# Kernel optimization log

Measured on AMD Instinct MI355X. Metric: run time of the kernel, lower is better.

## Reference

```python
import jax, jax.numpy as jnp
import numpy as np

N, E = 50000, 800000
IN_DIM, OUT_DIM, NHEAD = 256, 64, 4
SLOPE = 0.2
BN_EPS = 1e-5


def setup_inputs() -> dict:
    key = jax.random.key(0)
    ks = jax.random.split(key, 12)
    HD = NHEAD * OUT_DIM
    s = 1.0 / np.sqrt(IN_DIM)
    inp = {
        'feat': jax.random.normal(ks[0], (N, IN_DIM), dtype=jnp.float32),
        'src': jax.random.randint(ks[1], (E,), 0, N, dtype=jnp.int32),
        'dst': jax.random.randint(ks[2], (E,), 0, N, dtype=jnp.int32),
        # GATv2Conv params (DGL: separate src/dst linear, per-head attn vector, output bias)
        'W_src': jax.random.normal(ks[3], (IN_DIM, HD), dtype=jnp.float32) * s,
        'b_src': jnp.zeros((HD,), dtype=jnp.float32),
        'W_dst': jax.random.normal(ks[4], (IN_DIM, HD), dtype=jnp.float32) * s,
        'b_dst': jnp.zeros((HD,), dtype=jnp.float32),
        'attn': jax.random.normal(ks[5], (NHEAD, OUT_DIM), dtype=jnp.float32) * (1.0 / np.sqrt(OUT_DIM)),
        'out_bias': jnp.zeros((HD,), dtype=jnp.float32),
        # trailing fc: Linear(HD -> OUT_DIM) + BatchNorm1d + LeakyReLU (dropout = identity in eval)
        'fc_W': jax.random.normal(ks[6], (HD, OUT_DIM), dtype=jnp.float32) * (1.0 / np.sqrt(HD)),
        'fc_b': jnp.zeros((OUT_DIM,), dtype=jnp.float32),
        'gamma': jnp.ones((OUT_DIM,), dtype=jnp.float32),
        'beta': jnp.zeros((OUT_DIM,), dtype=jnp.float32),
    }
    return inp


def _leaky(x):
    return jnp.where(x >= 0, x, SLOPE * x)


def reference(feat, src, dst, W_src, b_src, W_dst, b_dst, attn, out_bias, fc_W, fc_b, gamma, beta):
    H, D = NHEAD, OUT_DIM
    h_src = (feat @ W_src + b_src).reshape(N, H, D)
    h_dst = (feat @ W_dst + b_dst).reshape(N, H, D)
    # per-edge GATv2 score: attn . LeakyReLU(h_src[u] + h_dst[v])
    hs_e = h_src[src]                                   # [E,H,D]
    e = jnp.einsum('ehd,hd->eh', _leaky(hs_e + h_dst[dst]), attn)  # [E,H]
    # segment softmax over incoming edges of each dst node
    m = jax.ops.segment_max(e, dst, num_segments=N)     # [N,H]
    ex = jnp.exp(e - m[dst])
    denom = jax.ops.segment_sum(ex, dst, num_segments=N)
    a = ex / denom[dst]                                 # [E,H]
    # weighted scatter-add aggregation
    rst = jax.ops.segment_sum(a[:, :, None] * hs_e, dst, num_segments=N)  # [N,H,D]
    rst = rst + out_bias.reshape(H, D)
    # trailing fc + BatchNorm1d (batch stats) + LeakyReLU
    z = rst.reshape(N, H * D) @ fc_W + fc_b
    mu = jnp.mean(z, axis=0)
    var = jnp.var(z, axis=0)
    z = (z - mu) * jax.lax.rsqrt(var + BN_EPS) * gamma + beta
    return _leaky(z)
```

## Files before the change

kernel.cpp:

```cpp
#include <hip/hip_runtime.h>
#include <math.h>

#define N_NODES 50000
#define N_EDGES 800000
#define HD 256
#define OUT_DIM 64
#define NHEAD 4
#define SLOPE 0.2f
#define BN_EPS 1e-5f
#define LOG2E 1.4426950408889634f
#define NTILES 391
#define HIST_BLOCKS 96

typedef __attribute__((ext_vector_type(8))) short short8;
typedef __attribute__((ext_vector_type(4))) float float4v;

__device__ __forceinline__ float leaky(float x) { return x >= 0.f ? x : SLOPE * x; }

__device__ __forceinline__ float bf2f(unsigned short u) {
    return __uint_as_float(((unsigned)u) << 16);
}
__device__ __forceinline__ unsigned short f2bf(float f) {
    unsigned u = __float_as_uint(f);
    unsigned r = (u + 0x7fffu + ((u >> 16) & 1u)) >> 16;
    return (unsigned short)r;
}

__device__ __forceinline__ short8 pack8(const float4 a, const float4 b) {
    short8 r;
    r[0] = (short)f2bf(a.x); r[1] = (short)f2bf(a.y);
    r[2] = (short)f2bf(a.z); r[3] = (short)f2bf(a.w);
    r[4] = (short)f2bf(b.x); r[5] = (short)f2bf(b.y);
    r[6] = (short)f2bf(b.z); r[7] = (short)f2bf(b.w);
    return r;
}

template <int CTRL>
__device__ __forceinline__ float ror_add(float v) {
    const int r = __builtin_amdgcn_update_dpp(0, __float_as_int(v), CTRL, 0xF, 0xF, true);
    return v + __int_as_float(r);
}
__device__ __forceinline__ float group16_sum(float v) {
    v = ror_add<0x121>(v);
    v = ror_add<0x122>(v);
    v = ror_add<0x124>(v);
    v = ror_add<0x128>(v);
    return v;
}

__global__ __launch_bounds__(256) void prep_kernel(const float* __restrict__ W_src,
                                                   const float* __restrict__ W_dst,
                                                   const float* __restrict__ fc_W,
                                                   unsigned short* __restrict__ WtS,
                                                   unsigned short* __restrict__ WtD,
                                                   unsigned short* __restrict__ WtF,
                                                   int* __restrict__ cnt2,
                                                   float* __restrict__ sums,
                                                   int* __restrict__ done) {
    const int b = blockIdx.x;
    const int t = threadIdx.x;
    if (b < 256) {
        WtS[(size_t)b * 256 + t] = f2bf(W_src[(size_t)t * 256 + b]);
    } else if (b < 512) {
        const int n = b - 256;
        WtD[(size_t)n * 256 + t] = f2bf(W_dst[(size_t)t * 256 + n]);
    } else if (b < 576) {
        const int n = b - 512;
        WtF[(size_t)n * 256 + t] = f2bf(fc_W[(size_t)t * 64 + n]);
    } else if (b < 674) {
        const int i = (b - 576) * 256 + t;
        if (i < 25000) ((int4*)cnt2)[i] = make_int4(0, 0, 0, 0);
    } else {
        if (t < 128) sums[t] = 0.f;
        if (t == 128) done[0] = 0;
    }
}

__global__ __launch_bounds__(256) void proj_kernel(const float* __restrict__ feat,
                                                   const unsigned short* __restrict__ BtS,
                                                   const unsigned short* __restrict__ BtD,
                                                   const float* __restrict__ bS,
                                                   const float* __restrict__ bD,
                                                   unsigned short* __restrict__ CS,
                                                   unsigned short* __restrict__ CD,
                                                   const int* __restrict__ dst,
                                                   int* __restrict__ cnt) {
    __shared__ unsigned short Bs[64 * 256];

    if (blockIdx.x < HIST_BLOCKS) {
        for (int i = blockIdx.x * 256 + threadIdx.x; i < N_EDGES; i += HIST_BLOCKS * 256)
            atomicAdd(&cnt[dst[i]], 1);
        return;
    }

    const int tile = blockIdx.x - HIST_BLOCKS;
    if (tile >= NTILES) return;

    const int t    = threadIdx.x;
    const int w    = t >> 6;
    const int lane = t & 63;
    const int q    = lane >> 4;
    const int l16  = lane & 15;

    const int m0 = tile * 128;

    int ar0 = m0 + w * 32 + l16;
    int ar1 = ar0 + 16;
    if (ar0 > N_NODES - 1) ar0 = N_NODES - 1;
    if (ar1 > N_NODES - 1) ar1 = N_NODES - 1;
    const float* Af0 = feat + (size_t)ar0 * 256 + q * 8;
    const float* Af1 = feat + (size_t)ar1 * 256 + q * 8;
    short8 afr0[8], afr1[8];
#pragma unroll
    for (int kk = 0; kk < 8; ++kk) {
        const float4 x0 = *(const float4*)(Af0 + kk * 32);
        const float4 y0 = *(const float4*)(Af0 + kk * 32 + 4);
        const float4 x1 = *(const float4*)(Af1 + kk * 32);
        const float4 y1 = *(const float4*)(Af1 + kk * 32 + 4);
        afr0[kk] = pack8(x0, y0);
        afr1[kk] = pack8(x1, y1);
    }

    const int r   = t >> 2;
    const int seg = t & 3;
    const int cc  = r >> 4;
    const int L   = r & 15;

    const int la8 = lane * 8;
    const int lsw[4] = {la8, la8 ^ 16, la8 ^ 32, la8 ^ 48};

    for (int ph = 0; ph < 8; ++ph) {
        const bool isD = (ph >= 4);
        const int  c0  = (ph & 3) * 64;
        const unsigned short* Bt   = isD ? BtD : BtS;
        const float*          bias = isD ? bD  : bS;
        unsigned short*       C    = isD ? CD  : CS;

        __syncthreads();
        {
            const unsigned short* g = Bt + (size_t)(c0 + r) * 256 + seg * 64;
#pragma unroll
            for (int kk2 = 0; kk2 < 2; ++kk2) {
                const int kk   = seg * 2 + kk2;
                const int c8kk = cc * 8 + kk;
                const int key  = ((c8kk >> 1) & 3) << 4;
#pragma unroll
                for (int q2 = 0; q2 < 4; ++q2)
                    *(short8*)(&Bs[((c8kk * 64 + q2 * 16 + L) * 8) ^ key]) =
                        *(const short8*)(g + kk2 * 32 + q2 * 8);
            }
        }
        __syncthreads();

        float vb[4];
#pragma unroll
        for (int c = 0; c < 4; ++c) vb[c] = bias[c0 + c * 16 + l16];

        float4v a0[4] = {}, a1[4] = {};
#pragma unroll
        for (int kk = 0; kk < 8; ++kk) {
            const short8 af0 = afr0[kk];
            const short8 af1 = afr1[kk];
#pragma unroll
            for (int c = 0; c < 4; ++c) {
                const int c8kk = c * 8 + kk;
                const short8 b = *(const short8*)(&Bs[c8kk * 512 + lsw[(c8kk >> 1) & 3]]);
                a0[c] = __builtin_amdgcn_mfma_f32_16x16x32_bf16(af0, b, a0[c], 0, 0, 0);
                a1[c] = __builtin_amdgcn_mfma_f32_16x16x32_bf16(af1, b, a1[c], 0, 0, 0);
            }
        }

        __syncthreads();
        unsigned short* Cw = Bs + w * 2304;
#pragma unroll
        for (int c = 0; c < 4; ++c) {
            const int cl = c * 16 + l16;
#pragma unroll
            for (int i = 0; i < 4; ++i) {
                Cw[(q * 4 + i) * 72 + cl]      = f2bf(a0[c][i] + vb[c]);
                Cw[(q * 4 + i + 16) * 72 + cl] = f2bf(a1[c][i] + vb[c]);
            }
        }
#pragma unroll
        for (int j = 0; j < 4; ++j) {
            const int rl = j * 8 + (lane >> 3);
            const short8 v = *(const short8*)(Cw + rl * 72 + (lane & 7) * 8);
            const int rg = m0 + w * 32 + rl;
            if (rg < N_NODES)
                *(short8*)(&C[(size_t)rg * 256 + c0 + (lane & 7) * 8]) = v;
        }
    }
}

__global__ __launch_bounds__(256) void fc_bn_kernel(const unsigned short* __restrict__ A,
                                                    const unsigned short* __restrict__ Bt,
                                                    const float* __restrict__ bias,
                                                    float* __restrict__ C,
                                                    float* __restrict__ sums,
                                                    int M) {
    const int w    = threadIdx.x >> 6;
    const int lane = threadIdx.x & 63;
    const int q    = lane >> 4;
    const int l16  = lane & 15;
    const int m0   = blockIdx.x * 64;
    const int t    = threadIdx.x;

    __shared__ float ssum[64], ssq[64];
    if (t < 64) { ssum[t] = 0.f; ssq[t] = 0.f; }

    int arow = m0 + w * 16 + l16;
    if (arow > M - 1) arow = M - 1;
    const unsigned short* Ab  = A  + (size_t)arow * 256 + q * 8;
    const unsigned short* Btb = Bt + (size_t)l16 * 256 + q * 8;

    float4v acc[4] = {};

    for (int k0 = 0; k0 < 256; k0 += 32) {
        const short8 af = *(const short8*)(Ab + k0);
#pragma unroll
        for (int c = 0; c < 4; ++c) {
            const short8 bf = *(const short8*)(Btb + (size_t)c * 16 * 256 + k0);
            acc[c] = __builtin_amdgcn_mfma_f32_16x16x32_bf16(af, bf, acc[c], 0, 0, 0);
        }
    }
    __syncthreads();

#pragma unroll
    for (int c = 0; c < 4; ++c) {
        const int col = c * 16 + l16;
        const float b = bias[col];
        float s = 0.f, qq = 0.f;
#pragma unroll
        for (int i = 0; i < 4; ++i) {
            const int r = m0 + w * 16 + q * 4 + i;
            if (r < M) {
                const float v = acc[c][i] + b;
                C[(size_t)r * 64 + col] = v;
                s += v;
                qq += v * v;
            }
        }
        atomicAdd(&ssum[col], s);
        atomicAdd(&ssq[col], qq);
    }
    __syncthreads();
    if (t < 64) {
        atomicAdd(&sums[t], ssum[t]);
        atomicAdd(&sums[64 + t], ssq[t]);
    }
}

__global__ __launch_bounds__(512) void scan_kernel(const int* __restrict__ cnt,
                                                   int* __restrict__ offs,
                                                   int* __restrict__ bsum,
                                                   int* __restrict__ bpre,
                                                   int* __restrict__ done) {
    __shared__ int s[512];
    __shared__ bool amLast;
    const int t = threadIdx.x;
    const int i = blockIdx.x * 512 + t;
    const int v = (i < N_NODES) ? cnt[i] : 0;
    s[t] = v;
    __syncthreads();
    for (int off = 1; off < 512; off <<= 1) {
        const int x = (t >= off) ? s[t - off] : 0;
        __syncthreads();
        s[t] += x;
        __syncthreads();
    }
    if (i < N_NODES) offs[i] = s[t] - v;
    if (t == 511) {
        bsum[blockIdx.x] = s[511];
        __threadfence();
        amLast = (atomicAdd(done, 1) == (int)gridDim.x - 1);
    }
    __syncthreads();
    if (amLast) {
        const int v2 = (t < (int)gridDim.x) ? atomicAdd(&bsum[t], 0) : 0;
        s[t] = v2;
        __syncthreads();
        for (int off = 1; off < 512; off <<= 1) {
            const int x = (t >= off) ? s[t - off] : 0;
            __syncthreads();
            s[t] += x;
            __syncthreads();
        }
        if (t < (int)gridDim.x) bpre[t] = s[t] - v2;
    }
}

__global__ void scatter_kernel(const int* __restrict__ src,
                               const int* __restrict__ dst,
                               const int* __restrict__ offs,
                               const int* __restrict__ bpre,
                               int* __restrict__ cursor,
                               int* __restrict__ srcl) {
    const int i = blockIdx.x * 256 + threadIdx.x;
    if (i < N_EDGES) {
        const int d = dst[i];
        const int p = offs[d] + bpre[d >> 9] + atomicAdd(&cursor[d], 1);
        srcl[p] = src[i];
    }
}

__global__ __launch_bounds__(256) void agg_fused_kernel(const unsigned short* __restrict__ h_src,
                                                        const unsigned short* __restrict__ h_dst,
                                                        const int* __restrict__ srcl,
                                                        const int* __restrict__ offs,
                                                        const int* __restrict__ bpre,
                                                        const float* __restrict__ attn,
                                                        const float* __restrict__ out_bias,
                                                        unsigned short* __restrict__ rst) {
    const int node = blockIdx.x * 4 + (threadIdx.x >> 6);
    const int lane = threadIdx.x & 63;
    const int d4 = lane * 4;

    const int beg = offs[node] + bpre[node >> 9];
    const int end = (node + 1 == N_NODES) ? N_EDGES
                                          : (offs[node + 1] + bpre[(node + 1) >> 9]);

    const uint2 hdu = *(const uint2*)(h_dst + (size_t)node * 256 + d4);
    const float hd0 = __uint_as_float(hdu.x << 16);
    const float hd1 = __uint_as_float(hdu.x & 0xffff0000u);
    const float hd2 = __uint_as_float(hdu.y << 16);
    const float hd3 = __uint_as_float(hdu.y & 0xffff0000u);

    const float4 araw = *(const float4*)(attn + d4);
    const float c10 = araw.x * (0.6f * LOG2E), c20 = araw.x * (0.4f * LOG2E);
    const float c11 = araw.y * (0.6f * LOG2E), c21 = araw.y * (0.4f * LOG2E);
    const float c12 = araw.z * (0.6f * LOG2E), c22 = araw.z * (0.4f * LOG2E);
    const float c13 = araw.w * (0.6f * LOG2E), c23 = araw.w * (0.4f * LOG2E);

    float wsum = 0.f, a0 = 0.f, a1 = 0.f, a2 = 0.f, a3 = 0.f;

#define EDGE_BODY(sreg)                                                          \
    {                                                                            \
        const unsigned short* row = h_src + (size_t)(sreg) * 256;                \
        const uint2 u = *(const uint2*)(row + d4);                               \
        const float r0 = __uint_as_float(u.x << 16);                             \
        const float r1 = __uint_as_float(u.x & 0xffff0000u);                     \
        const float r2 = __uint_as_float(u.y << 16);                             \
        const float r3 = __uint_as_float(u.y & 0xffff0000u);                     \
        const float y0 = r0 + hd0, y1 = r1 + hd1, y2 = r2 + hd2, y3 = r3 + hd3;  \
        float pp = fmaf(c10, y0, c20 * __builtin_fabsf(y0));                     \
        pp = fmaf(c11, y1, fmaf(c21, __builtin_fabsf(y1), pp));                  \
        pp = fmaf(c12, y2, fmaf(c22, __builtin_fabsf(y2), pp));                  \
        pp = fmaf(c13, y3, fmaf(c23, __builtin_fabsf(y3), pp));                  \
        pp = group16_sum(pp);                                                    \
        const float wg = __builtin_amdgcn_exp2f(pp);                             \
        wsum += wg;                                                              \
        a0 = fmaf(wg, r0, a0);                                                   \
        a1 = fmaf(wg, r1, a1);                                                   \
        a2 = fmaf(wg, r2, a2);                                                   \
        a3 = fmaf(wg, r3, a3);                                                   \
    }

    int p = beg;
    const int nfull = (end - beg) >> 2;
    for (int it = 0; it < nfull; ++it, p += 4) {
        const int s0 = __builtin_amdgcn_readfirstlane(srcl[p]);
        const int s1 = __builtin_amdgcn_readfirstlane(srcl[p + 1]);
        const int s2 = __builtin_amdgcn_readfirstlane(srcl[p + 2]);
        const int s3 = __builtin_amdgcn_readfirstlane(srcl[p + 3]);
        EDGE_BODY(s0);
        EDGE_BODY(s1);
        EDGE_BODY(s2);
        EDGE_BODY(s3);
    }
    for (; p < end; ++p) {
        const int s0 = __builtin_amdgcn_readfirstlane(srcl[p]);
        EDGE_BODY(s0);
    }
#undef EDGE_BODY

    const float inv = (wsum > 0.f) ? 1.f / wsum : 0.f;
    const float4 ob = *(const float4*)(out_bias + d4);
    ushort4 o;
    o.x = f2bf(fmaf(a0, inv, ob.x));
    o.y = f2bf(fmaf(a1, inv, ob.y));
    o.z = f2bf(fmaf(a2, inv, ob.z));
    o.w = f2bf(fmaf(a3, inv, ob.w));
    *(ushort4*)(rst + (size_t)node * 256 + d4) = o;
}

__global__ __launch_bounds__(256) void bn_final_kernel(float* __restrict__ z,
                                                       const float* __restrict__ sums,
                                                       const float* __restrict__ gamma,
                                                       const float* __restrict__ beta) {
    const int i = blockIdx.x * 256 + threadIdx.x;
    if (i < N_NODES * 16) {
        const int c4 = (i & 15) * 4;
        float4 v = ((const float4*)z)[i];
        float out[4] = {v.x, v.y, v.z, v.w};
#pragma unroll
        for (int j = 0; j < 4; ++j) {
            const int col = c4 + j;
            const float mu  = sums[col] * (1.f / N_NODES);
            const float var = sums[64 + col] * (1.f / N_NODES) - mu * mu;
            const float sc  = rsqrtf(var + BN_EPS) * gamma[col];
            const float sh  = beta[col] - mu * sc;
            out[j] = leaky(fmaf(out[j], sc, sh));
        }
        ((float4*)z)[i] = make_float4(out[0], out[1], out[2], out[3]);
    }
}

extern "C" void kernel_launch(void* const* d_in, const int* in_sizes, int n_in,
                              void* d_out, int out_size, void* d_ws, size_t ws_size,
                              hipStream_t stream) {
    const float* feat    = (const float*)d_in[0];
    const int*   src     = (const int*)  d_in[1];
    const int*   dst     = (const int*)  d_in[2];
    const float* W_src   = (const float*)d_in[3];
    const float* b_src   = (const float*)d_in[4];
    const float* W_dst   = (const float*)d_in[5];
    const float* b_dst   = (const float*)d_in[6];
    const float* attn    = (const float*)d_in[7];
    const float* out_bias= (const float*)d_in[8];
    const float* fc_W    = (const float*)d_in[9];
    const float* fc_b    = (const float*)d_in[10];
    const float* gamma   = (const float*)d_in[11];
    const float* beta    = (const float*)d_in[12];
    float* z = (float*)d_out;

    char* ws = (char*)d_ws;
    size_t off = 0;
    auto carve = [&](size_t bytes) -> void* {
        void* p = ws + off;
        off = (off + bytes + 255) & ~(size_t)255;
        return p;
    };
    unsigned short* h_src_bf= (unsigned short*)carve((size_t)N_NODES * 256 * 2);
    unsigned short* h_dst_bf= (unsigned short*)carve((size_t)N_NODES * 256 * 2);
    unsigned short* rst_bf  = (unsigned short*)carve((size_t)N_NODES * 256 * 2);
    unsigned short* WtS     = (unsigned short*)carve((size_t)256 * 256 * 2);
    unsigned short* WtD     = (unsigned short*)carve((size_t)256 * 256 * 2);
    unsigned short* WtF     = (unsigned short*)carve((size_t)64 * 256 * 2);
    int*   srcl   = (int*)  carve((size_t)N_EDGES * 4);
    int*   cnt    = (int*)  carve((size_t)2 * N_NODES * 4);
    int*   cursor = cnt + N_NODES;
    int*   offs   = (int*)  carve((size_t)(N_NODES + 1) * 4);
    int*   bsum   = (int*)  carve(128 * 4);
    int*   bpre   = (int*)  carve(128 * 4);
    float* sums   = (float*)carve(128 * 4);
    int*   done   = (int*)  carve(64);

    const int nchunks = (N_NODES + 511) / 512;

    prep_kernel<<<675, 256, 0, stream>>>(W_src, W_dst, fc_W,
                                         WtS, WtD, WtF, cnt, sums, done);

    proj_kernel<<<HIST_BLOCKS + NTILES, 256, 0, stream>>>(
        feat, WtS, WtD, b_src, b_dst, h_src_bf, h_dst_bf, dst, cnt);

    scan_kernel<<<nchunks, 512, 0, stream>>>(cnt, offs, bsum, bpre, done);
    scatter_kernel<<<(N_EDGES + 255) / 256, 256, 0, stream>>>(src, dst, offs, bpre, cursor, srcl);

    agg_fused_kernel<<<N_NODES / 4, 256, 0, stream>>>(h_src_bf, h_dst_bf, srcl, offs, bpre,
                                                      attn, out_bias, rst_bf);

    fc_bn_kernel<<<(N_NODES + 63) / 64, 256, 0, stream>>>(rst_bf, WtF, fc_b, z, sums, N_NODES);

    bn_final_kernel<<<(N_NODES * 16 + 255) / 256, 256, 0, stream>>>(z, sums, gamma, beta);
}
```

Before: 311.6 us.

## Process two edges per wavefront with 16-byte loads in aggregation kernel

```diff
diff --git a/kernel.cpp b/kernel.cpp
--- a/kernel.cpp
+++ b/kernel.cpp
@@ -40,11 +40,10 @@
     const int r = __builtin_amdgcn_update_dpp(0, __float_as_int(v), CTRL, 0xF, 0xF, true);
     return v + __int_as_float(r);
 }
-__device__ __forceinline__ float group16_sum(float v) {
-    v = ror_add<0x121>(v);
-    v = ror_add<0x122>(v);
-    v = ror_add<0x124>(v);
-    v = ror_add<0x128>(v);
+__device__ __forceinline__ float group8_sum(float v) {
+    v = ror_add<0x141>(v);
+    v = ror_add<0x4E>(v);
+    v = ror_add<0xB1>(v);
     return v;
 }
 
@@ -313,74 +312,110 @@
                                                         unsigned short* __restrict__ rst) {
     const int node = blockIdx.x * 4 + (threadIdx.x >> 6);
     const int lane = threadIdx.x & 63;
-    const int d4 = lane * 4;
+    const int l32  = lane & 31;
+    const bool hiH = (lane >= 32);
+    const int d8   = l32 * 8;
 
     const int beg = offs[node] + bpre[node >> 9];
     const int end = (node + 1 == N_NODES) ? N_EDGES
                                           : (offs[node + 1] + bpre[(node + 1) >> 9]);
 
-    const uint2 hdu = *(const uint2*)(h_dst + (size_t)node * 256 + d4);
-    const float hd0 = __uint_as_float(hdu.x << 16);
-    const float hd1 = __uint_as_float(hdu.x & 0xffff0000u);
-    const float hd2 = __uint_as_float(hdu.y << 16);
-    const float hd3 = __uint_as_float(hdu.y & 0xffff0000u);
-
-    const float4 araw = *(const float4*)(attn + d4);
-    const float c10 = araw.x * (0.6f * LOG2E), c20 = araw.x * (0.4f * LOG2E);
-    const float c11 = araw.y * (0.6f * LOG2E), c21 = araw.y * (0.4f * LOG2E);
-    const float c12 = araw.z * (0.6f * LOG2E), c22 = araw.z * (0.4f * LOG2E);
-    const float c13 = araw.w * (0.6f * LOG2E), c23 = araw.w * (0.4f * LOG2E);
-
-    float wsum = 0.f, a0 = 0.f, a1 = 0.f, a2 = 0.f, a3 = 0.f;
-
-#define EDGE_BODY(sreg)                                                          \
+    float hd[8];
+    {
+        const uint4 u = *(const uint4*)(h_dst + (size_t)node * 256 + d8);
+        hd[0] = __uint_as_float(u.x << 16); hd[1] = __uint_as_float(u.x & 0xffff0000u);
+        hd[2] = __uint_as_float(u.y << 16); hd[3] = __uint_as_float(u.y & 0xffff0000u);
+        hd[4] = __uint_as_float(u.z << 16); hd[5] = __uint_as_float(u.z & 0xffff0000u);
+        hd[6] = __uint_as_float(u.w << 16); hd[7] = __uint_as_float(u.w & 0xffff0000u);
+    }
+    float c1[8], c2[8];
+    {
+        const float4 a0 = *(const float4*)(attn + d8);
+        const float4 a1 = *(const float4*)(attn + d8 + 4);
+        const float k1 = 0.6f * LOG2E, k2 = 0.4f * LOG2E;
+        c1[0] = a0.x * k1; c2[0] = a0.x * k2;
+        c1[1] = a0.y * k1; c2[1] = a0.y * k2;
+        c1[2] = a0.z * k1; c2[2] = a0.z * k2;
+        c1[3] = a0.w * k1; c2[3] = a0.w * k2;
+        c1[4] = a1.x * k1; c2[4] = a1.x * k2;
+        c1[5] = a1.y * k1; c2[5] = a1.y * k2;
+        c1[6] = a1.z * k1; c2[6] = a1.z * k2;
+        c1[7] = a1.w * k1; c2[7] = a1.w * k2;
+    }
+
+    float wsum = 0.f;
+    float acc[8] = {0.f, 0.f, 0.f, 0.f, 0.f, 0.f, 0.f, 0.f};
+
+#define EDGE_PAIR(sA, sB, msk)                                                   \
     {                                                                            \
-        const unsigned short* row = h_src + (size_t)(sreg) * 256;                \
-        const uint2 u = *(const uint2*)(row + d4);                               \
-        const float r0 = __uint_as_float(u.x << 16);                             \
-        const float r1 = __uint_as_float(u.x & 0xffff0000u);                     \
-        const float r2 = __uint_as_float(u.y << 16);                             \
-        const float r3 = __uint_as_float(u.y & 0xffff0000u);                     \
-        const float y0 = r0 + hd0, y1 = r1 + hd1, y2 = r2 + hd2, y3 = r3 + hd3;  \
-        float pp = fmaf(c10, y0, c20 * __builtin_fabsf(y0));                     \
-        pp = fmaf(c11, y1, fmaf(c21, __builtin_fabsf(y1), pp));                  \
-        pp = fmaf(c12, y2, fmaf(c22, __builtin_fabsf(y2), pp));                  \
-        pp = fmaf(c13, y3, fmaf(c23, __builtin_fabsf(y3), pp));                  \
-        pp = group16_sum(pp);                                                    \
-        const float wg = __builtin_amdgcn_exp2f(pp);                             \
+        const int ssel = hiH ? (sB) : (sA);                                      \
+        const uint4 u = *(const uint4*)(h_src + (size_t)ssel * 256 + d8);        \
+        float r[8];                                                              \
+        r[0] = __uint_as_float(u.x << 16); r[1] = __uint_as_float(u.x & 0xffff0000u); \
+        r[2] = __uint_as_float(u.y << 16); r[3] = __uint_as_float(u.y & 0xffff0000u); \
+        r[4] = __uint_as_float(u.z << 16); r[5] = __uint_as_float(u.z & 0xffff0000u); \
+        r[6] = __uint_as_float(u.w << 16); r[7] = __uint_as_float(u.w & 0xffff0000u); \
+        float pp = 0.f;                                                          \
+        _Pragma("unroll")                                                        \
+        for (int j = 0; j < 8; ++j) {                                            \
+            const float y = r[j] + hd[j];                                        \
+            pp = fmaf(c1[j], y, fmaf(c2[j], __builtin_fabsf(y), pp));            \
+        }                                                                        \
+        pp = group8_sum(pp);                                                     \
+        const float wg = __builtin_amdgcn_exp2f(pp) * (msk);                     \
         wsum += wg;                                                              \
-        a0 = fmaf(wg, r0, a0);                                                   \
-        a1 = fmaf(wg, r1, a1);                                                   \
-        a2 = fmaf(wg, r2, a2);                                                   \
-        a3 = fmaf(wg, r3, a3);                                                   \
+        _Pragma("unroll")                                                        \
+        for (int j = 0; j < 8; ++j) acc[j] = fmaf(wg, r[j], acc[j]);             \
     }
 
     int p = beg;
-    const int nfull = (end - beg) >> 2;
-    for (int it = 0; it < nfull; ++it, p += 4) {
+    const int npairs = (end - beg) >> 1;
+    const int nf4 = npairs >> 2;
+    for (int it = 0; it < nf4; ++it, p += 8) {
         const int s0 = __builtin_amdgcn_readfirstlane(srcl[p]);
         const int s1 = __builtin_amdgcn_readfirstlane(srcl[p + 1]);
         const int s2 = __builtin_amdgcn_readfirstlane(srcl[p + 2]);
         const int s3 = __builtin_amdgcn_readfirstlane(srcl[p + 3]);
-        EDGE_BODY(s0);
-        EDGE_BODY(s1);
-        EDGE_BODY(s2);
-        EDGE_BODY(s3);
-    }
-    for (; p < end; ++p) {
+        const int s4 = __builtin_amdgcn_readfirstlane(srcl[p + 4]);
+        const int s5 = __builtin_amdgcn_readfirstlane(srcl[p + 5]);
+        const int s6 = __builtin_amdgcn_readfirstlane(srcl[p + 6]);
+        const int s7 = __builtin_amdgcn_readfirstlane(srcl[p + 7]);
+        EDGE_PAIR(s0, s1, 1.f);
+        EDGE_PAIR(s2, s3, 1.f);
+        EDGE_PAIR(s4, s5, 1.f);
+        EDGE_PAIR(s6, s7, 1.f);
+    }
+    for (int rp = nf4 * 4; rp < npairs; ++rp, p += 2) {
         const int s0 = __builtin_amdgcn_readfirstlane(srcl[p]);
-        EDGE_BODY(s0);
-    }
-#undef EDGE_BODY
+        const int s1 = __builtin_amdgcn_readfirstlane(srcl[p + 1]);
+        EDGE_PAIR(s0, s1, 1.f);
+    }
+    if ((end - beg) & 1) {
+        const float hm = hiH ? 0.f : 1.f;
+        const int s0 = __builtin_amdgcn_readfirstlane(srcl[p]);
+        EDGE_PAIR(s0, s0, hm);
+    }
+#undef EDGE_PAIR
+
+    wsum += __shfl_xor(wsum, 32, 64);
+#pragma unroll
+    for (int j = 0; j < 8; ++j) acc[j] += __shfl_xor(acc[j], 32, 64);
 
     const float inv = (wsum > 0.f) ? 1.f / wsum : 0.f;
-    const float4 ob = *(const float4*)(out_bias + d4);
-    ushort4 o;
-    o.x = f2bf(fmaf(a0, inv, ob.x));
-    o.y = f2bf(fmaf(a1, inv, ob.y));
-    o.z = f2bf(fmaf(a2, inv, ob.z));
-    o.w = f2bf(fmaf(a3, inv, ob.w));
-    *(ushort4*)(rst + (size_t)node * 256 + d4) = o;
+    if (!hiH) {
+        const float4 ob0 = *(const float4*)(out_bias + d8);
+        const float4 ob1 = *(const float4*)(out_bias + d8 + 4);
+        short8 o;
+        o[0] = (short)f2bf(fmaf(acc[0], inv, ob0.x));
+        o[1] = (short)f2bf(fmaf(acc[1], inv, ob0.y));
+        o[2] = (short)f2bf(fmaf(acc[2], inv, ob0.z));
+        o[3] = (short)f2bf(fmaf(acc[3], inv, ob0.w));
+        o[4] = (short)f2bf(fmaf(acc[4], inv, ob1.x));
+        o[5] = (short)f2bf(fmaf(acc[5], inv, ob1.y));
+        o[6] = (short)f2bf(fmaf(acc[6], inv, ob1.z));
+        o[7] = (short)f2bf(fmaf(acc[7], inv, ob1.w));
+        *(short8*)(&rst[(size_t)node * 256 + d8]) = o;
+    }
 }
 
 __global__ __launch_bounds__(256) void bn_final_kernel(float* __restrict__ z,
```

After: 310.5 us. No clear change (-0.4%).

## Split projection GEMM across two launches to overlap with histogram and scatter

Applied to the files above, without the earlier changes.

```diff
diff --git a/kernel.cpp b/kernel.cpp
--- a/kernel.cpp
+++ b/kernel.cpp
@@ -11,6 +11,8 @@
 #define LOG2E 1.4426950408889634f
 #define NTILES 391
 #define HIST_BLOCKS 96
+#define SPLIT_A 192
+#define SCAT_BLOCKS 3125
 
 typedef __attribute__((ext_vector_type(8))) short short8;
 typedef __attribute__((ext_vector_type(4))) float float4v;
@@ -76,26 +78,15 @@
     }
 }
 
-__global__ __launch_bounds__(256) void proj_kernel(const float* __restrict__ feat,
-                                                   const unsigned short* __restrict__ BtS,
-                                                   const unsigned short* __restrict__ BtD,
-                                                   const float* __restrict__ bS,
-                                                   const float* __restrict__ bD,
-                                                   unsigned short* __restrict__ CS,
-                                                   unsigned short* __restrict__ CD,
-                                                   const int* __restrict__ dst,
-                                                   int* __restrict__ cnt) {
-    __shared__ unsigned short Bs[64 * 256];
-
-    if (blockIdx.x < HIST_BLOCKS) {
-        for (int i = blockIdx.x * 256 + threadIdx.x; i < N_EDGES; i += HIST_BLOCKS * 256)
-            atomicAdd(&cnt[dst[i]], 1);
-        return;
-    }
-
-    const int tile = blockIdx.x - HIST_BLOCKS;
-    if (tile >= NTILES) return;
-
+__device__ __forceinline__ void proj_tile(int tile,
+                                          const float* __restrict__ feat,
+                                          const unsigned short* __restrict__ BtS,
+                                          const unsigned short* __restrict__ BtD,
+                                          const float* __restrict__ bS,
+                                          const float* __restrict__ bD,
+                                          unsigned short* __restrict__ CS,
+                                          unsigned short* __restrict__ CD,
+                                          unsigned short* Bs) {
     const int t    = threadIdx.x;
     const int w    = t >> 6;
     const int lane = t & 63;
@@ -190,6 +181,56 @@
                 *(short8*)(&C[(size_t)rg * 256 + c0 + (lane & 7) * 8]) = v;
         }
     }
+}
+
+__global__ __launch_bounds__(256) void projA_kernel(const float* __restrict__ feat,
+                                                    const unsigned short* __restrict__ BtS,
+                                                    const unsigned short* __restrict__ BtD,
+                                                    const float* __restrict__ bS,
+                                                    const float* __restrict__ bD,
+                                                    unsigned short* __restrict__ CS,
+                                                    unsigned short* __restrict__ CD,
+                                                    const int* __restrict__ dst,
+                                                    int* __restrict__ cnt) {
+    __shared__ unsigned short Bs[64 * 256];
+
+    if (blockIdx.x < HIST_BLOCKS) {
+        for (int i = blockIdx.x * 256 + threadIdx.x; i < N_EDGES; i += HIST_BLOCKS * 256)
+            atomicAdd(&cnt[dst[i]], 1);
+        return;
+    }
+    const int tile = blockIdx.x - HIST_BLOCKS;
+    if (tile >= SPLIT_A) return;
+    proj_tile(tile, feat, BtS, BtD, bS, bD, CS, CD, Bs);
+}
+
+__global__ __launch_bounds__(256) void projB_kernel(const float* __restrict__ feat,
+                                                    const unsigned short* __restrict__ BtS,
+                                                    const unsigned short* __restrict__ BtD,
+                                                    const float* __restrict__ bS,
+                                                    const float* __restrict__ bD,
+                                                    unsigned short* __restrict__ CS,
+                                                    unsigned short* __restrict__ CD,
+                                                    const int* __restrict__ src,
+                                                    const int* __restrict__ dst,
+                                                    const int* __restrict__ offs,
+                                                    const int* __restrict__ bpre,
+                                                    int* __restrict__ cursor,
+                                                    int* __restrict__ srcl) {
+    __shared__ unsigned short Bs[64 * 256];
+
+    if (blockIdx.x < SCAT_BLOCKS) {
+        const int i = blockIdx.x * 256 + threadIdx.x;
+        if (i < N_EDGES) {
+            const int d = dst[i];
+            const int p = offs[d] + bpre[d >> 9] + atomicAdd(&cursor[d], 1);
+            srcl[p] = src[i];
+        }
+        return;
+    }
+    const int tile = SPLIT_A + (blockIdx.x - SCAT_BLOCKS);
+    if (tile >= NTILES) return;
+    proj_tile(tile, feat, BtS, BtD, bS, bD, CS, CD, Bs);
 }
 
 __global__ __launch_bounds__(256) void fc_bn_kernel(const unsigned short* __restrict__ A,
@@ -286,20 +327,6 @@
             __syncthreads();
         }
         if (t < (int)gridDim.x) bpre[t] = s[t] - v2;
-    }
-}
-
-__global__ void scatter_kernel(const int* __restrict__ src,
-                               const int* __restrict__ dst,
-                               const int* __restrict__ offs,
-                               const int* __restrict__ bpre,
-                               int* __restrict__ cursor,
-                               int* __restrict__ srcl) {
-    const int i = blockIdx.x * 256 + threadIdx.x;
-    if (i < N_EDGES) {
-        const int d = dst[i];
-        const int p = offs[d] + bpre[d >> 9] + atomicAdd(&cursor[d], 1);
-        srcl[p] = src[i];
     }
 }
 
@@ -450,11 +477,14 @@
     prep_kernel<<<675, 256, 0, stream>>>(W_src, W_dst, fc_W,
                                          WtS, WtD, WtF, cnt, sums, done);
 
-    proj_kernel<<<HIST_BLOCKS + NTILES, 256, 0, stream>>>(
+    projA_kernel<<<HIST_BLOCKS + SPLIT_A, 256, 0, stream>>>(
         feat, WtS, WtD, b_src, b_dst, h_src_bf, h_dst_bf, dst, cnt);
 
     scan_kernel<<<nchunks, 512, 0, stream>>>(cnt, offs, bsum, bpre, done);
-    scatter_kernel<<<(N_EDGES + 255) / 256, 256, 0, stream>>>(src, dst, offs, bpre, cursor, srcl);
+
+    projB_kernel<<<SCAT_BLOCKS + (NTILES - SPLIT_A), 256, 0, stream>>>(
+        feat, WtS, WtD, b_src, b_dst, h_src_bf, h_dst_bf,
+        src, dst, offs, bpre, cursor, srcl);
 
     agg_fused_kernel<<<N_NODES / 4, 256, 0, stream>>>(h_src_bf, h_dst_bf, srcl, offs, bpre,
                                                       attn, out_bias, rst_bf);
```

Result: slower. 345.6 us (+10.9%).
